# Kernel tuning notes

Hardware: AMD Instinct MI355X
Metric: run time of the kernel (lower is better)

## Reference

```python
import jax, jax.numpy as jnp
import numpy as np

B, S, D, H = 1, 1024, 1024, 16
DR, DV, R = 64, 64, 256          # rope head dim, v head dim, kv_lora_rank (qk_nope_head_dim = 0)
V, L, E, F, TOPK = 32000, 2, 4, 4096, 2
EPS, THETA, LB_WEIGHT = 1e-6, 10000.0, 0.01
SCALE = DR ** -0.5               # q_head_dim = nope(0) + rope(64)


def rms_norm(x, w):
    return x * jax.lax.rsqrt(jnp.mean(x * x, axis=-1, keepdims=True) + EPS) * w


def rotate_half(x):
    h = x.shape[-1] // 2
    return jnp.concatenate([-x[..., h:], x[..., :h]], axis=-1)


def apply_rope(x, cos, sin):
    # DeepSeek-V3 rotary: interleaved->half reorder, then rotate-half
    *lead, d = x.shape
    x = x.reshape(*lead, d // 2, 2).swapaxes(-1, -2).reshape(*lead, d)
    return x * cos + rotate_half(x) * sin


def setup_inputs() -> dict:
    key = jax.random.key(0)
    ks = iter(jax.random.split(key, 40))
    w = lambda shape: (0.02 * jax.random.normal(next(ks), shape)).astype(jnp.float32)
    return dict(
        tokens=jax.random.randint(next(ks), (B, S), 0, V, dtype=jnp.int32),
        embed=w((V, D)),                      # tied embedding / lm_head
        q_w=w((L, H * DR, D)),                # q_proj (q_lora_rank=None)
        kva_w=w((L, R + DR, D)),              # kv_a_proj_with_mqa
        kva_ln=jnp.ones((L, R), jnp.float32), # kv_a_layernorm (RMSNorm)
        kvb_w=w((L, H * DV, R)),              # kv_b_proj (nope=0 -> values only)
        o_w=w((L, D, H * DV)),
        norm1_w=jnp.ones((L, D), jnp.float32),
        norm2_w=jnp.ones((L, D), jnp.float32),
        router_w=w((L, E, D)),
        router_b=jnp.zeros((L, E), jnp.float32),
        w1=w((L, E, D, F)),
        b1=jnp.zeros((L, E, F), jnp.float32),
        w2=w((L, E, F, D)),
        b2=jnp.zeros((L, E, D), jnp.float32),
        final_norm_w=jnp.ones((D,), jnp.float32),
    )


def _layer(x, p, cos, sin, mask):
    # --- MLHA attention (DeepSeek-V3, qk_nope=0 => keys are shared rope k_pe) ---
    h = rms_norm(x, p['norm1_w'])
    q = (h @ p['q_w'].T).reshape(B, S, H, DR).transpose(0, 2, 1, 3)        # [B,H,S,DR]
    kva = h @ p['kva_w'].T                                                 # [B,S,R+DR]
    ckv, k_pe = kva[..., :R], kva[..., R:]
    v = (rms_norm(ckv, p['kva_ln']) @ p['kvb_w'].T).reshape(B, S, H, DV).transpose(0, 2, 1, 3)
    q = apply_rope(q, cos[None, None], sin[None, None])
    k = apply_rope(k_pe[:, None], cos[None, None], sin[None, None])[:, 0]  # [B,S,DR] shared across heads
    scores = jnp.einsum('bhsd,btd->bhst', q, k) * SCALE + mask
    attn = jax.nn.softmax(scores, axis=-1)
    o = jnp.einsum('bhst,bhtd->bhsd', attn, v).transpose(0, 2, 1, 3).reshape(B, S, H * DV)
    x = x + o @ p['o_w'].T
    # --- MoE FFN (top-k routing, renormalized gates, switch-style aux loss) ---
    h2 = rms_norm(x, p['norm2_w']).reshape(B * S, D)
    probs = jax.nn.softmax(h2 @ p['router_w'].T + p['router_b'], axis=-1)  # [T,E]
    topv, topi = jax.lax.top_k(probs, TOPK)
    gates = topv / jnp.sum(topv, axis=-1, keepdims=True)
    sel = jax.nn.one_hot(topi, E, dtype=probs.dtype)                       # [T,K,E]
    combine = jnp.einsum('tke,tk->te', sel, gates)                         # [T,E]
    hmid = jax.nn.gelu(jnp.einsum('td,edf->tef', h2, p['w1']) + p['b1'], approximate=False)
    y = jnp.einsum('tef,efd->ted', hmid, p['w2']) + p['b2']                # [T,E,D]
    ff = jnp.einsum('te,ted->td', combine, y).reshape(B, S, D)
    frac = jnp.mean(jnp.max(sel, axis=1), axis=0)                          # token fraction per expert
    aux = E * jnp.sum(frac * jnp.mean(probs, axis=0))
    return x + ff, aux


def reference(tokens, embed, q_w, kva_w, kva_ln, kvb_w, o_w, norm1_w, norm2_w,
              router_w, router_b, w1, b1, w2, b2, final_norm_w):
    x = embed[tokens]                                                      # [B,S,D]
    inv = 1.0 / (THETA ** (jnp.arange(0, DR, 2, dtype=jnp.float32) / DR))
    freqs = jnp.arange(S, dtype=jnp.float32)[:, None] * inv[None, :]
    emb = jnp.concatenate([freqs, freqs], axis=-1)
    cos, sin = jnp.cos(emb), jnp.sin(emb)                                  # [S,DR]
    mask = jnp.where(jnp.triu(jnp.ones((S, S), bool), 1), -jnp.inf, 0.0)[None, None]
    stacked = dict(q_w=q_w, kva_w=kva_w, kva_ln=kva_ln, kvb_w=kvb_w, o_w=o_w,
                   norm1_w=norm1_w, norm2_w=norm2_w, router_w=router_w, router_b=router_b,
                   w1=w1, b1=b1, w2=w2, b2=b2)

    def step(carry, p):
        x, aux = carry
        x, a = _layer(x, p, cos, sin, mask)
        return (x, aux + a), None

    (x, aux), _ = jax.lax.scan(step, (x, jnp.float32(0.0)), stacked)
    x = rms_norm(x, final_norm_w)
    logits = x @ embed.T                                                   # tied lm_head
    return logits, aux * LB_WEIGHT
```

## Files before the change

kernel.cpp:

```cpp
#include <hip/hip_runtime.h>
#include <hip/hip_bf16.h>
#include <math.h>

typedef __hip_bfloat16 bf16;
typedef __attribute__((ext_vector_type(8))) short short8;
typedef __attribute__((ext_vector_type(4))) short short4v;
typedef __attribute__((ext_vector_type(4))) float f32x4;

static constexpr int SEQ  = 1024;
static constexpr int DIM  = 1024;
static constexpr int NH   = 16;
static constexpr int DRR  = 64;
static constexpr int RR   = 256;
static constexpr int KVAN = RR + DRR;
static constexpr int VOC  = 32000;
static constexpr int NEXP = 4;
static constexpr int FFD  = 4096;
static constexpr int NSLOT = SEQ*2;
static constexpr float EPSF = 1e-6f;
static constexpr float ATT_SCALE = 0.125f;
static constexpr float LBW = 0.01f;

__device__ __forceinline__ bool is_bf(const uint32_t* mg){ return *mg == 0x3F803F80u; }
__device__ __forceinline__ float ldin(const void* p, size_t i, bool bf){
  return bf ? __bfloat162float(((const bf16*)p)[i]) : ((const float*)p)[i];
}
__device__ __forceinline__ short f2bs(float f){
  bf16 h = __float2bfloat16(f);
  return *reinterpret_cast<short*>(&h);
}
__device__ __forceinline__ void split2(float a, short& hi, short& lo){
  bf16 h = __float2bfloat16(a);
  hi = *reinterpret_cast<short*>(&h);
  lo = f2bs(a - __bfloat162float(h));
}

__device__ __forceinline__ void gload16(const short* gp, short* lp){
  __builtin_amdgcn_global_load_lds(
      (const __attribute__((address_space(1))) void*)gp,
      (__attribute__((address_space(3))) void*)lp, 16, 0, 0);
}

__device__ __forceinline__ void stage64(const short* __restrict__ g, int ldg,
    short* lds, int w, int lane){
  const int rA = lane >> 3;
  const int ss = (lane & 7) ^ rA;
  #pragma unroll
  for (int j = 0; j < 2; ++j){
    const int row = w*16 + j*8 + rA;
    gload16(g + (size_t)row*ldg + ss*8, lds + (w*16 + j*8)*64);
  }
}

__device__ __forceinline__ float blk_sum256(float v, float* red){
  const int tid = threadIdx.x;
  red[tid] = v; __syncthreads();
  for (int o = 128; o > 0; o >>= 1){
    if (tid < o) red[tid] += red[tid + o];
    __syncthreads();
  }
  float r = red[0]; __syncthreads();
  return r;
}
__device__ __forceinline__ float blk_max256(float v, float* red){
  const int tid = threadIdx.x;
  red[tid] = v; __syncthreads();
  for (int o = 128; o > 0; o >>= 1){
    if (tid < o) red[tid] = fmaxf(red[tid], red[tid + o]);
    __syncthreads();
  }
  float r = red[0]; __syncthreads();
  return r;
}

__global__ __launch_bounds__(256) void k_embed(const int* __restrict__ tok,
    const void* __restrict__ emb, float* __restrict__ x, const uint32_t* mg){
  const bool bf = is_bf(mg);
  const int t = blockIdx.x;
  const int id = tok[t];
  for (int d = threadIdx.x; d < DIM; d += 256)
    x[(size_t)t*DIM + d] = ldin(emb, (size_t)id*DIM + d, bf);
}

__global__ void k_ropetab(float* __restrict__ cosb, float* __restrict__ sinb){
  const int t = blockIdx.x, i = threadIdx.x;
  float inv = powf(10000.0f, -(float)i / 32.0f);
  float fr = (float)t * inv;
  cosb[t*32 + i] = cosf(fr);
  sinb[t*32 + i] = sinf(fr);
}

__global__ __launch_bounds__(256) void k_rmsnorm(const float* __restrict__ in, int instride,
    const void* __restrict__ w, size_t wofs, float* __restrict__ out, int outstride,
    int dim, const uint32_t* mg){
  __shared__ float red[256];
  const bool bf = is_bf(mg);
  const int t = blockIdx.x;
  const float* row = in + (size_t)t*instride;
  float ss = 0.f;
  for (int d = threadIdx.x; d < dim; d += 256){ float v = row[d]; ss = fmaf(v, v, ss); }
  float tot = blk_sum256(ss, red);
  float rs = rsqrtf(tot / (float)dim + EPSF);
  float* orow = out + (size_t)t*outstride;
  for (int d = threadIdx.x; d < dim; d += 256)
    orow[d] = row[d] * rs * ldin(w, wofs + d, bf);
}

__global__ __launch_bounds__(256) void k_split2_act(const float* __restrict__ X,
    short* __restrict__ S, int K, int total){
  const int i = (blockIdx.x*256 + threadIdx.x)*8;
  if (i >= total) return;
  const int row = i / K, col = i - row*K;
  const float4 v0 = *(const float4*)&X[i];
  const float4 v1 = *(const float4*)&X[i+4];
  const float vv[8] = {v0.x,v0.y,v0.z,v0.w,v1.x,v1.y,v1.z,v1.w};
  short8 h, l;
  #pragma unroll
  for (int q = 0; q < 8; ++q){ short a,b; split2(vv[q], a, b); h[q]=a; l[q]=b; }
  const size_t base = (size_t)row*2*K + col;
  *(short8*)&S[base] = h;
  *(short8*)&S[base + K] = l;
}

__global__ __launch_bounds__(256) void k_split2_wt(const void* __restrict__ W, size_t wofs,
    short* __restrict__ S, int K, int total, const uint32_t* mg){
  const bool bf = is_bf(mg);
  const int i = (blockIdx.x*256 + threadIdx.x)*8;
  if (i >= total) return;
  const int row = i / K, col = i - row*K;
  float vv[8];
  if (!bf){
    const float* Wf = (const float*)W + wofs;
    const float4 v0 = *(const float4*)&Wf[i];
    const float4 v1 = *(const float4*)&Wf[i+4];
    vv[0]=v0.x; vv[1]=v0.y; vv[2]=v0.z; vv[3]=v0.w;
    vv[4]=v1.x; vv[5]=v1.y; vv[6]=v1.z; vv[7]=v1.w;
  } else {
    #pragma unroll
    for (int q = 0; q < 8; ++q) vv[q] = __bfloat162float(((const bf16*)W)[wofs + i + q]);
  }
  short8 h, l;
  #pragma unroll
  for (int q = 0; q < 8; ++q){ short a,b; split2(vv[q], a, b); h[q]=a; l[q]=b; }
  const size_t base = (size_t)row*2*K + col;
  *(short8*)&S[base] = h;
  *(short8*)&S[base + K] = l;
}

__global__ __launch_bounds__(256) void k_split_hi(const void* __restrict__ W,
    short* __restrict__ Wh, int total, const uint32_t* mg){
  const bool bf = is_bf(mg);
  const int i = (blockIdx.x*256 + threadIdx.x)*8;
  if (i >= total) return;
  float vv[8];
  if (!bf){
    const float* Wf = (const float*)W;
    const float4 v0 = *(const float4*)&Wf[i];
    const float4 v1 = *(const float4*)&Wf[i+4];
    vv[0]=v0.x; vv[1]=v0.y; vv[2]=v0.z; vv[3]=v0.w;
    vv[4]=v1.x; vv[5]=v1.y; vv[6]=v1.z; vv[7]=v1.w;
  } else {
    #pragma unroll
    for (int q = 0; q < 8; ++q) vv[q] = __bfloat162float(((const bf16*)W)[i + q]);
  }
  short8 h;
  #pragma unroll
  for (int q = 0; q < 8; ++q) h[q] = f2bs(vv[q]);
  *(short8*)&Wh[i] = h;
}

template<int WLO>
__global__ __launch_bounds__(256) void k_transp2v(const void* __restrict__ B, size_t bofs,
    size_t perexp, short* __restrict__ S, int K, int N, const uint32_t* mg){
  __shared__ float t[64][65];
  const bool bf = is_bf(mg);
  const int e = blockIdx.z;
  const int n0 = blockIdx.x*64, k0 = blockIdx.y*64;
  const size_t src = bofs + (size_t)e*perexp;
  const int tid = threadIdx.x;
  const int rr = tid >> 4, cc = (tid & 15) * 4;
  if (!bf){
    const float* Bf = (const float*)B + src;
    #pragma unroll
    for (int p = 0; p < 4; ++p){
      const int r = rr + p*16;
      const float4 v = *(const float4*)&Bf[(size_t)(k0+r)*N + n0 + cc];
      t[r][cc+0] = v.x; t[r][cc+1] = v.y; t[r][cc+2] = v.z; t[r][cc+3] = v.w;
    }
  } else {
    #pragma unroll
    for (int p = 0; p < 4; ++p){
      const int r = rr + p*16;
      #pragma unroll
      for (int q = 0; q < 4; ++q)
        t[r][cc+q] = __bfloat162float(((const bf16*)B)[src + (size_t)(k0+r)*N + n0 + cc + q]);
    }
  }
  __syncthreads();
  const int nn = tid >> 2, ks = (tid & 3) * 16;
  const size_t dst = (size_t)e*(size_t)N*2*K + (size_t)(n0+nn)*2*K + k0 + ks;
  short8 h0, h1, l0, l1;
  #pragma unroll
  for (int q = 0; q < 8; ++q){
    short a, b;
    split2(t[ks+q][nn], a, b);      h0[q] = a; l0[q] = b;
    split2(t[ks+8+q][nn], a, b);    h1[q] = a; l1[q] = b;
  }
  *(short8*)&S[dst]     = h0;
  *(short8*)&S[dst + 8] = h1;
  if (WLO){
    *(short8*)&S[dst + K]     = l0;
    *(short8*)&S[dst + K + 8] = l1;
  }
}

__global__ __launch_bounds__(256) void k_gather2(const float* __restrict__ h2,
    const int* __restrict__ tos, short* __restrict__ S){
  const int slot = blockIdx.x, tid = threadIdx.x;
  const int t = tos[slot];
  const int i = tid*4;
  const float4 v = *(const float4*)&h2[(size_t)t*DIM + i];
  const float vv[4] = {v.x, v.y, v.z, v.w};
  short4v h, l;
  #pragma unroll
  for (int q = 0; q < 4; ++q){ short a,b; split2(vv[q], a, b); h[q]=a; l[q]=b; }
  *(short4v*)&S[(size_t)slot*2*DIM + i] = h;
  *(short4v*)&S[(size_t)slot*2*DIM + DIM + i] = l;
}

__device__ __forceinline__ void tg_stage(const short* __restrict__ A, int lda, int ac,
    const short* __restrict__ B, int ldb, int bc, int bm, int bn,
    short* sA, short* sB, int wid, int rA, int ss){
  #pragma unroll
  for (int j = 0; j < 4; ++j){
    const int row = wid*32 + j*8 + rA;
    gload16(A + (size_t)(bm+row)*lda + ac + ss*8, sA + (wid*32 + j*8)*64);
    gload16(B + (size_t)(bn+row)*ldb + bc + ss*8, sB + (wid*32 + j*8)*64);
  }
}

#define TG_MFMAS(sAp, sBp)                                                      \
    _Pragma("unroll")                                                           \
    for (int kk = 0; kk < 2; ++kk){                                             \
      short8 a[4], b[4];                                                        \
      _Pragma("unroll")                                                         \
      for (int f = 0; f < 4; ++f){                                              \
        const int ar = wr*64 + f*16 + lr;                                       \
        a[f] = *(const short8*)&(sAp)[ar*64 + (((kk*4+lks)^(ar&7)))*8];         \
        const int br = wc*64 + f*16 + lr;                                       \
        b[f] = *(const short8*)&(sBp)[br*64 + (((kk*4+lks)^(br&7)))*8];         \
      }                                                                         \
      _Pragma("unroll")                                                         \
      for (int f = 0; f < 4; ++f)                                               \
        _Pragma("unroll")                                                       \
        for (int g = 0; g < 4; ++g)                                             \
          acc[f*4+g] = __builtin_amdgcn_mfma_f32_16x16x32_bf16(                 \
              a[f], b[g], acc[f*4+g], 0, 0, 0);                                 \
    }

#define TG_KADDR(st)                                                            \
  const int kt = (st)*64;                                                       \
  const int t = (kt >= 2*K) ? 2 : (kt >= K) ? 1 : 0;                            \
  const int ko = kt - t*K;                                                      \
  const int ac = ko + ((t == 2) ? K : 0);                                       \
  const int bc = ko + ((t == 1) ? K : 0);

template<int MODE>
__global__ __launch_bounds__(256) void k_tgemm_wt(
    const short* __restrict__ A, int lda,
    const short* __restrict__ W, int ldb, int K, int nt,
    float* __restrict__ C, int N, int S, float* __restrict__ Cpart){
  __shared__ alignas(16) short sA[128*64];
  __shared__ alignas(16) short sB[128*64];
  const int tid = threadIdx.x;
  const int wid = tid >> 6, lane = tid & 63;
  const int wr = wid >> 1, wc = wid & 1;
  const int bm = blockIdx.y * 128, bn = blockIdx.x * 128;
  const int rA = lane >> 3, ss = (lane & 7) ^ rA;
  const int lr = lane & 15, lks = lane >> 4;
  f32x4 acc[16];
  #pragma unroll
  for (int i = 0; i < 16; ++i) acc[i] = f32x4{0,0,0,0};

  const int nsteps = (nt*K) >> 6;
  const int per = (nsteps + S - 1)/S;
  const int st0 = blockIdx.z*per, st1 = min(nsteps, st0 + per);
  for (int st = st0; st < st1; ++st){
    TG_KADDR(st)
    tg_stage(A, lda, ac, W, ldb, bc, bm, bn, sA, sB, wid, rA, ss);
    __syncthreads();
    TG_MFMAS(sA, sB)
    __syncthreads();
  }
  const int r4 = lks*4, cj = lr;
  if (S == 1){
    #pragma unroll
    for (int f = 0; f < 4; ++f)
      #pragma unroll
      for (int g = 0; g < 4; ++g)
        #pragma unroll
        for (int r = 0; r < 4; ++r){
          const int gm = bm + wr*64 + f*16 + r4 + r;
          const int gn = bn + wc*64 + g*16 + cj;
          if (gn >= N) continue;
          const size_t idx = (size_t)gm*N + gn;
          if (MODE == 0) C[idx] = acc[f*4+g][r];
          else           C[idx] += acc[f*4+g][r];
        }
  } else {
    const int M = gridDim.y * 128;
    float* P = Cpart + (size_t)blockIdx.z*M*N;
    #pragma unroll
    for (int f = 0; f < 4; ++f)
      #pragma unroll
      for (int g = 0; g < 4; ++g)
        #pragma unroll
        for (int r = 0; r < 4; ++r){
          const int gm = bm + wr*64 + f*16 + r4 + r;
          const int gn = bn + wc*64 + g*16 + cj;
          if (gn >= N) continue;
          P[(size_t)gm*N + gn] = acc[f*4+g][r];
        }
  }
}

__global__ __launch_bounds__(256) void k_tgemm_wtL(
    const short* __restrict__ A, int lda,
    const short* __restrict__ W, int ldb, int K,
    float* __restrict__ C, int N){
  __shared__ alignas(16) short sA[2][128*64];
  __shared__ alignas(16) short sB[2][128*64];
  const int tid = threadIdx.x;
  const int wid = tid >> 6, lane = tid & 63;
  const int wr = wid >> 1, wc = wid & 1;
  const int T = gridDim.x * gridDim.y;
  const int p = blockIdx.x + gridDim.x * blockIdx.y;
  const int u = (p & 7) * (T >> 3) + (p >> 3);
  const int bn = (u >> 3) * 128;
  const int bm = (u & 7) * 128;
  const int rA = lane >> 3, ss = (lane & 7) ^ rA;
  const int lr = lane & 15, lks = lane >> 4;
  f32x4 acc[16];
  #pragma unroll
  for (int i = 0; i < 16; ++i) acc[i] = f32x4{0,0,0,0};

  const int nsteps = K >> 6;
  tg_stage(A, lda, 0, W, ldb, 0, bm, bn, sA[0], sB[0], wid, rA, ss);
  asm volatile("s_waitcnt vmcnt(0)" ::: "memory");
  __builtin_amdgcn_s_barrier();
  int cur = 0;
  for (int st = 0; st < nsteps; ++st){
    const bool pf = (st + 1 < nsteps);
    if (pf){
      const int ko = (st + 1)*64;
      tg_stage(A, lda, ko, W, ldb, ko, bm, bn, sA[cur^1], sB[cur^1], wid, rA, ss);
    }
    __builtin_amdgcn_s_setprio(1);
    TG_MFMAS(sA[cur], sB[cur])
    __builtin_amdgcn_s_setprio(0);
    if (pf){
      asm volatile("s_waitcnt vmcnt(0)" ::: "memory");
      __builtin_amdgcn_s_barrier();
      cur ^= 1;
    }
  }
  const int r4 = lks*4, cj = lr;
  #pragma unroll
  for (int f = 0; f < 4; ++f)
    #pragma unroll
    for (int g = 0; g < 4; ++g)
      #pragma unroll
      for (int r = 0; r < 4; ++r){
        const int gm = bm + wr*64 + f*16 + r4 + r;
        const int gn = bn + wc*64 + g*16 + cj;
        if (gn >= N) continue;
        C[(size_t)gm*N + gn] = acc[f*4+g][r];
      }
}

template<int MODE>
__global__ __launch_bounds__(256) void k_redw(const float* __restrict__ Cpart,
    float* __restrict__ C, int total, int S){
  const int i = blockIdx.x*256 + threadIdx.x;
  if (i >= total) return;
  float v = 0.f;
  for (int s = 0; s < S; ++s) v += Cpart[(size_t)s*total + i];
  if (MODE == 0) C[i] = v;
  else           C[i] += v;
}

template<int ACT, int OSPLIT>
__global__ __launch_bounds__(256) void k_tgemm_grp(
    const short* __restrict__ A, int lda,
    const short* __restrict__ Wall, int ldb, int K, int nt,
    const void* __restrict__ bias, size_t biofs, size_t perexp_bias,
    float* __restrict__ Cf, short* __restrict__ Cs,
    const int* __restrict__ meta, int N, const uint32_t* mg,
    int S, float* __restrict__ Cpart){
  __shared__ alignas(16) short sA[2][128*64];
  __shared__ alignas(16) short sB[2][128*64];
  const bool bf = is_bf(mg);
  const int e = blockIdx.z / S, zs = blockIdx.z - e*S;
  const int cnt = meta[e], off = meta[NEXP + e];
  const int r0 = blockIdx.y * 128;
  if (r0 >= cnt) return;
  const int rows_valid = min(128, cnt - r0);
  const int bm = off + r0, bn = blockIdx.x * 128;
  const short* W = Wall + (size_t)e*(size_t)N*ldb;
  const size_t bib = biofs + (size_t)e * perexp_bias;

  const int tid = threadIdx.x;
  const int wid = tid >> 6, lane = tid & 63;
  const int wr = wid >> 1, wc = wid & 1;
  const int rA = lane >> 3, ss = (lane & 7) ^ rA;
  const int lr = lane & 15, lks = lane >> 4;
  f32x4 acc[16];
  #pragma unroll
  for (int i = 0; i < 16; ++i) acc[i] = f32x4{0,0,0,0};

  const int nsteps = (nt*K) >> 6;
  const int per = (nsteps + S - 1)/S;
  const int st0 = zs*per, st1 = min(nsteps, st0 + per);
  {
    TG_KADDR(st0)
    tg_stage(A, lda, ac, W, ldb, bc, bm, bn, sA[0], sB[0], wid, rA, ss);
    asm volatile("s_waitcnt vmcnt(0)" ::: "memory");
    __builtin_amdgcn_s_barrier();
  }
  int cur = 0;
  for (int st = st0; st < st1; ++st){
    const bool pf = (st + 1 < st1);
    if (pf){
      TG_KADDR(st+1)
      tg_stage(A, lda, ac, W, ldb, bc, bm, bn, sA[cur^1], sB[cur^1], wid, rA, ss);
    }
    __builtin_amdgcn_s_setprio(1);
    TG_MFMAS(sA[cur], sB[cur])
    __builtin_amdgcn_s_setprio(0);
    if (pf){
      asm volatile("s_waitcnt vmcnt(0)" ::: "memory");
      __builtin_amdgcn_s_barrier();
      cur ^= 1;
    }
  }
  const int r4 = lks*4, cj = lr;
  if (S == 1){
    #pragma unroll
    for (int f = 0; f < 4; ++f)
      #pragma unroll
      for (int g = 0; g < 4; ++g)
        #pragma unroll
        for (int r = 0; r < 4; ++r){
          const int rin = wr*64 + f*16 + r4 + r;
          if (rin >= rows_valid) continue;
          const int gn = bn + wc*64 + g*16 + cj;
          float v = acc[f*4+g][r] + ldin(bias, bib + gn, bf);
          if (ACT == 1) v = 0.5f * v * (1.f + erff(v * 0.70710678118654752f));
          if (OSPLIT){
            short hi, lo; split2(v, hi, lo);
            const size_t idx = (size_t)(bm + rin)*2*N + gn;
            Cs[idx] = hi; Cs[idx + N] = lo;
          } else {
            Cf[(size_t)(bm + rin)*N + gn] = v;
          }
        }
  } else {
    float* P = Cpart + (size_t)zs*NSLOT*N;
    #pragma unroll
    for (int f = 0; f < 4; ++f)
      #pragma unroll
      for (int g = 0; g < 4; ++g)
        #pragma unroll
        for (int r = 0; r < 4; ++r){
          const int rin = wr*64 + f*16 + r4 + r;
          if (rin >= rows_valid) continue;
          const int gn = bn + wc*64 + g*16 + cj;
          P[(size_t)(bm + rin)*N + gn] = acc[f*4+g][r];
        }
  }
}

template<int ACT, int OSPLIT>
__global__ __launch_bounds__(256) void k_tgemm_grpF(
    const short* __restrict__ A, int lda,
    const short* __restrict__ Wall, int ldb, int K,
    const void* __restrict__ bias, size_t biofs, size_t perexp_bias,
    float* __restrict__ Cf, short* __restrict__ Cs,
    const int* __restrict__ meta, int N, const uint32_t* mg,
    int S, float* __restrict__ Cpart){
  __shared__ alignas(16) short sAh[128*64];
  __shared__ alignas(16) short sAl[128*64];
  __shared__ alignas(16) short sBh[128*64];
  __shared__ alignas(16) short sBl[128*64];
  const bool bf = is_bf(mg);
  const int e = blockIdx.z / S, zs = blockIdx.z - e*S;
  const int cnt = meta[e], off = meta[NEXP + e];
  const int r0 = blockIdx.y * 128;
  if (r0 >= cnt) return;
  const int rows_valid = min(128, cnt - r0);
  const int bm = off + r0, bn = blockIdx.x * 128;
  const short* W = Wall + (size_t)e*(size_t)N*ldb;
  const size_t bib = biofs + (size_t)e * perexp_bias;

  const int tid = threadIdx.x;
  const int wid = tid >> 6, lane = tid & 63;
  const int wr = wid >> 1, wc = wid & 1;
  const int rA = lane >> 3, ss = (lane & 7) ^ rA;
  const int lr = lane & 15, lks = lane >> 4;
  f32x4 acc[16];
  #pragma unroll
  for (int i = 0; i < 16; ++i) acc[i] = f32x4{0,0,0,0};

  const int nsteps = K >> 6;
  const int per = (nsteps + S - 1)/S;
  const int st0 = zs*per, st1 = min(nsteps, st0 + per);
  for (int st = st0; st < st1; ++st){
    const int ko = st*64;
    #pragma unroll
    for (int j = 0; j < 4; ++j){
      const int row = wid*32 + j*8 + rA;
      const size_t arow = (size_t)(bm+row)*lda;
      const size_t brow = (size_t)(bn+row)*ldb;
      const int dst = (wid*32 + j*8)*64;
      gload16(A + arow + ko + ss*8,     sAh + dst);
      gload16(A + arow + K + ko + ss*8, sAl + dst);
      gload16(W + brow + ko + ss*8,     sBh + dst);
      gload16(W + brow + K + ko + ss*8, sBl + dst);
    }
    __syncthreads();
    __builtin_amdgcn_s_setprio(1);
    TG_MFMAS(sAh, sBh)
    TG_MFMAS(sAh, sBl)
    TG_MFMAS(sAl, sBh)
    __builtin_amdgcn_s_setprio(0);
    __syncthreads();
  }
  const int r4 = lks*4, cj = lr;
  if (S == 1){
    #pragma unroll
    for (int f = 0; f < 4; ++f)
      #pragma unroll
      for (int g = 0; g < 4; ++g)
        #pragma unroll
        for (int r = 0; r < 4; ++r){
          const int rin = wr*64 + f*16 + r4 + r;
          if (rin >= rows_valid) continue;
          const int gn = bn + wc*64 + g*16 + cj;
          float v = acc[f*4+g][r] + ldin(bias, bib + gn, bf);
          if (ACT == 1) v = 0.5f * v * (1.f + erff(v * 0.70710678118654752f));
          if (OSPLIT){
            short hi, lo; split2(v, hi, lo);
            const size_t idx = (size_t)(bm + rin)*2*N + gn;
            Cs[idx] = hi; Cs[idx + N] = lo;
          } else {
            Cf[(size_t)(bm + rin)*N + gn] = v;
          }
        }
  } else {
    float* P = Cpart + (size_t)zs*NSLOT*N;
    #pragma unroll
    for (int f = 0; f < 4; ++f)
      #pragma unroll
      for (int g = 0; g < 4; ++g)
        #pragma unroll
        for (int r = 0; r < 4; ++r){
          const int rin = wr*64 + f*16 + r4 + r;
          if (rin >= rows_valid) continue;
          const int gn = bn + wc*64 + g*16 + cj;
          P[(size_t)(bm + rin)*N + gn] = acc[f*4+g][r];
        }
  }
}

template<int ACT, int OSPLIT>
__global__ __launch_bounds__(256) void k_redg(const float* __restrict__ Cpart, int S,
    const int* __restrict__ eid,
    const void* __restrict__ bias, size_t biofs, size_t perexp_bias,
    float* __restrict__ Cf, short* __restrict__ Cs, int N, const uint32_t* mg){
  const bool bf = is_bf(mg);
  const int slot = blockIdx.x;
  const int e = eid[slot];
  const size_t bib = biofs + (size_t)e * perexp_bias;
  for (int n = threadIdx.x; n < N; n += 256){
    float v = 0.f;
    for (int s = 0; s < S; ++s)
      v += Cpart[(size_t)s*NSLOT*N + (size_t)slot*N + n];
    v += ldin(bias, bib + n, bf);
    if (ACT == 1) v = 0.5f * v * (1.f + erff(v * 0.70710678118654752f));
    if (OSPLIT){
      short hi, lo; split2(v, hi, lo);
      const size_t idx = (size_t)slot*2*N + n;
      Cs[idx] = hi; Cs[idx + N] = lo;
    } else {
      Cf[(size_t)slot*N + n] = v;
    }
  }
}

__global__ __launch_bounds__(512) void k_ropeq2(const float* __restrict__ qraw,
    const float* __restrict__ cosb, const float* __restrict__ sinb,
    short* __restrict__ Qsp){
  const int t = blockIdx.x, tid = threadIdx.x;
  const int hh = tid >> 5, i = tid & 31;
  const size_t base = (size_t)t*DIM + hh*DRR;
  const float u0 = qraw[base + 2*i];
  const float u1 = qraw[base + 2*i + 1];
  const float c = cosb[t*32 + i], s = sinb[t*32 + i];
  const float o0 = u0*c - u1*s;
  const float o1 = u1*c + u0*s;
  short h0,l0,h1,l1;
  split2(o0,h0,l0); split2(o1,h1,l1);
  short* q = Qsp + ((size_t)hh*SEQ + t)*128;
  q[i] = h0;      q[64+i] = l0;
  q[i+32] = h1;   q[96+i] = l1;
}

__global__ void k_ropek2(const float* __restrict__ kva,
    const float* __restrict__ cosb, const float* __restrict__ sinb,
    short* __restrict__ Kb){
  const int t = blockIdx.x, i = threadIdx.x;
  const float u0 = kva[(size_t)t*KVAN + RR + 2*i];
  const float u1 = kva[(size_t)t*KVAN + RR + 2*i + 1];
  const float c = cosb[t*32 + i], s = sinb[t*32 + i];
  const float o0 = u0*c - u1*s;
  const float o1 = u1*c + u0*s;
  short h0,l0,h1,l1;
  split2(o0,h0,l0); split2(o1,h1,l1);
  short* k = Kb + (size_t)t*128;
  k[i] = h0;      k[64+i] = l0;
  k[i+32] = h1;   k[96+i] = l1;
}

__global__ __launch_bounds__(256) void k_vsplit(const float* __restrict__ vbuf,
    short* __restrict__ Vt){
  __shared__ float tbuf[32][33];
  const int kv0 = blockIdx.x*32, d0 = blockIdx.y*32;
  const int c = threadIdx.x & 31, rb = threadIdx.x >> 5;
  #pragma unroll
  for (int p = 0; p < 4; ++p){
    const int r = rb + p*8;
    tbuf[r][c] = vbuf[(size_t)(kv0 + r)*DIM + d0 + c];
  }
  __syncthreads();
  #pragma unroll
  for (int p = 0; p < 4; ++p){
    const int rr = rb + p*8;
    const int dg = d0 + rr;
    const int h = dg >> 6, dl = dg & 63;
    short hi, lo; split2(tbuf[c][rr], hi, lo);
    const size_t o = ((size_t)h*64 + dl)*2048 + kv0 + c;
    Vt[o] = hi; Vt[o + 1024] = lo;
  }
}

__global__ __launch_bounds__(256) void k_fattn(
    const short* __restrict__ Qsp, const short* __restrict__ Kb,
    const short* __restrict__ Vt, float* __restrict__ outb){
  __shared__ alignas(16) short Qsh[64*64], Qsl[64*64];
  __shared__ alignas(16) short Ksh[64*64], Ksl[64*64];
  __shared__ alignas(16) short Vsh[64*64], Vsl[64*64];
  __shared__ alignas(16) short Ph[64*64], Pl[64*64];
  const int qt = blockIdx.x, hh = blockIdx.y;
  const int qbase = qt*64;
  const int tid = threadIdx.x;
  const int w = tid >> 6, lane = tid & 63;
  const int lr = lane & 15, lks = lane >> 4;
  const int r4 = lks*4, cj = lr;

  stage64(Qsp + ((size_t)hh*SEQ + qbase)*128,      128, Qsh, w, lane);
  stage64(Qsp + ((size_t)hh*SEQ + qbase)*128 + 64, 128, Qsl, w, lane);

  float m_r[4], l_r[4], alpha[4], rmax[4], rsum[4];
  f32x4 o[4];
  #pragma unroll
  for (int r = 0; r < 4; ++r){ m_r[r] = -3.0e38f; l_r[r] = 0.f; }
  #pragma unroll
  for (int g = 0; g < 4; ++g) o[g] = f32x4{0,0,0,0};
  __syncthreads();

  for (int kt = 0; kt <= qt; ++kt){
    const int kvbase = kt*64;
    stage64(Kb + (size_t)kvbase*128,        128, Ksh, w, lane);
    stage64(Kb + (size_t)kvbase*128 + 64,   128, Ksl, w, lane);
    stage64(Vt + (size_t)hh*64*2048 + kvbase,        2048, Vsh, w, lane);
    stage64(Vt + (size_t)hh*64*2048 + 1024 + kvbase, 2048, Vsl, w, lane);
    __syncthreads();

    f32x4 s[4];
    #pragma unroll
    for (int g = 0; g < 4; ++g) s[g] = f32x4{0,0,0,0};
    #pragma unroll
    for (int term = 0; term < 3; ++term){
      const short* Ab = (term == 2) ? Qsl : Qsh;
      const short* Bb = (term == 1) ? Ksl : Ksh;
      #pragma unroll
      for (int ks = 0; ks < 2; ++ks){
        const int arow = w*16 + lr;
        const short8 a = *(const short8*)&Ab[arow*64 + (((ks*4+lks)^(arow&7))*8)];
        #pragma unroll
        for (int g = 0; g < 4; ++g){
          const int brow = g*16 + lr;
          const short8 b = *(const short8*)&Bb[brow*64 + (((ks*4+lks)^(brow&7))*8)];
          s[g] = __builtin_amdgcn_mfma_f32_16x16x32_bf16(a, b, s[g], 0, 0, 0);
        }
      }
    }
    #pragma unroll
    for (int r = 0; r < 4; ++r) rmax[r] = -3.0e38f;
    #pragma unroll
    for (int g = 0; g < 4; ++g)
      #pragma unroll
      for (int r = 0; r < 4; ++r){
        float v = s[g][r] * ATT_SCALE;
        if (kvbase + g*16 + cj > qbase + w*16 + r4 + r) v = -3.0e38f;
        s[g][r] = v;
        rmax[r] = fmaxf(rmax[r], v);
      }
    #pragma unroll
    for (int msk = 1; msk < 16; msk <<= 1)
      #pragma unroll
      for (int r = 0; r < 4; ++r)
        rmax[r] = fmaxf(rmax[r], __shfl_xor(rmax[r], msk));
    #pragma unroll
    for (int r = 0; r < 4; ++r){
      const float mn = fmaxf(m_r[r], rmax[r]);
      alpha[r] = expf(m_r[r] - mn);
      m_r[r] = mn;
      rsum[r] = 0.f;
    }
    #pragma unroll
    for (int g = 0; g < 4; ++g)
      #pragma unroll
      for (int r = 0; r < 4; ++r){
        const float p = expf(s[g][r] - m_r[r]);
        s[g][r] = p;
        rsum[r] += p;
      }
    #pragma unroll
    for (int msk = 1; msk < 16; msk <<= 1)
      #pragma unroll
      for (int r = 0; r < 4; ++r)
        rsum[r] += __shfl_xor(rsum[r], msk);
    #pragma unroll
    for (int r = 0; r < 4; ++r)
      l_r[r] = l_r[r]*alpha[r] + rsum[r];
    #pragma unroll
    for (int g = 0; g < 4; ++g)
      #pragma unroll
      for (int r = 0; r < 4; ++r)
        o[g][r] *= alpha[r];
    #pragma unroll
    for (int g = 0; g < 4; ++g)
      #pragma unroll
      for (int r = 0; r < 4; ++r){
        short hi, lo; split2(s[g][r], hi, lo);
        const int prow = w*16 + r4 + r;
        const int sl = g*2 + (cj >> 3);
        const int addr = prow*64 + ((sl ^ (prow & 7))*8) + (cj & 7);
        Ph[addr] = hi; Pl[addr] = lo;
      }
    #pragma unroll
    for (int term = 0; term < 3; ++term){
      const short* Ab = (term == 2) ? Pl : Ph;
      const short* Bb = (term == 1) ? Vsl : Vsh;
      #pragma unroll
      for (int ks = 0; ks < 2; ++ks){
        const int arow = w*16 + lr;
        const short8 a = *(const short8*)&Ab[arow*64 + (((ks*4+lks)^(arow&7))*8)];
        #pragma unroll
        for (int g = 0; g < 4; ++g){
          const int brow = g*16 + lr;
          const short8 b = *(const short8*)&Bb[brow*64 + (((ks*4+lks)^(brow&7))*8)];
          o[g] = __builtin_amdgcn_mfma_f32_16x16x32_bf16(a, b, o[g], 0, 0, 0);
        }
      }
    }
    __syncthreads();
  }
  #pragma unroll
  for (int g = 0; g < 4; ++g)
    #pragma unroll
    for (int r = 0; r < 4; ++r)
      outb[(size_t)(qbase + w*16 + r4 + r)*DIM + hh*64 + g*16 + cj] = o[g][r] / l_r[r];
}

template<int MODE>
__global__ __launch_bounds__(256) void k_mgemm_wt(const float* __restrict__ A,
    const void* __restrict__ W, size_t wofs, float* __restrict__ C,
    int M, int N, int K, const uint32_t* mg){
  __shared__ alignas(16) short As[64][40];
  __shared__ alignas(16) short Bs[64][40];
  const bool bf = is_bf(mg);
  const int tid = threadIdx.x;
  const int bm = blockIdx.x * 64, bn = blockIdx.y * 64;
  const int wid = tid >> 6, lane = tid & 63;
  const int wr = wid >> 1, wc = wid & 1;
  const int lrow = lane & 15, lk = (lane >> 4) * 8;
  const int srow = tid >> 3, sk = (tid & 7) * 4;
  f32x4 acc00{0,0,0,0}, acc01{0,0,0,0}, acc10{0,0,0,0}, acc11{0,0,0,0};
  for (int kt = 0; kt < K; kt += 32){
    #pragma unroll
    for (int p = 0; p < 2; ++p){
      const int r = srow + p*32;
      const size_t abase = (size_t)(bm + r)*K + kt + sk;
      As[r][sk+0] = f2bs(A[abase+0]);
      As[r][sk+1] = f2bs(A[abase+1]);
      As[r][sk+2] = f2bs(A[abase+2]);
      As[r][sk+3] = f2bs(A[abase+3]);
      const size_t wbase = wofs + (size_t)(bn + r)*K + kt + sk;
      Bs[r][sk+0] = f2bs(ldin(W, wbase+0, bf));
      Bs[r][sk+1] = f2bs(ldin(W, wbase+1, bf));
      Bs[r][sk+2] = f2bs(ldin(W, wbase+2, bf));
      Bs[r][sk+3] = f2bs(ldin(W, wbase+3, bf));
    }
    __syncthreads();
    const short8 a0 = *(const short8*)&As[wr*32 +      lrow][lk];
    const short8 a1 = *(const short8*)&As[wr*32 + 16 + lrow][lk];
    const short8 b0 = *(const short8*)&Bs[wc*32 +      lrow][lk];
    const short8 b1 = *(const short8*)&Bs[wc*32 + 16 + lrow][lk];
    acc00 = __builtin_amdgcn_mfma_f32_16x16x32_bf16(a0, b0, acc00, 0, 0, 0);
    acc01 = __builtin_amdgcn_mfma_f32_16x16x32_bf16(a0, b1, acc01, 0, 0, 0);
    acc10 = __builtin_amdgcn_mfma_f32_16x16x32_bf16(a1, b0, acc10, 0, 0, 0);
    acc11 = __builtin_amdgcn_mfma_f32_16x16x32_bf16(a1, b1, acc11, 0, 0, 0);
    __syncthreads();
  }
  const int r4 = (lane >> 4) * 4, cj = lane & 15;
  #pragma unroll
  for (int fm = 0; fm < 2; ++fm)
    #pragma unroll
    for (int fn = 0; fn < 2; ++fn){
      const f32x4 av = fm == 0 ? (fn == 0 ? acc00 : acc01) : (fn == 0 ? acc10 : acc11);
      #pragma unroll
      for (int r = 0; r < 4; ++r){
        const int gm = bm + wr*32 + fm*16 + r4 + r;
        const int gn = bn + wc*32 + fn*16 + cj;
        const size_t idx = (size_t)gm*N + gn;
        if (MODE == 0) C[idx] = av[r];
        else           C[idx] += av[r];
      }
    }
}

template<int ACT>
__global__ __launch_bounds__(256) void k_gemm_grp(const float* __restrict__ A,
    const void* __restrict__ B, size_t bofs, size_t perexp_b,
    const void* __restrict__ bias, size_t biofs, size_t perexp_bias,
    float* __restrict__ C, const int* __restrict__ meta,
    int N, int K, const uint32_t* mg){
  __shared__ float As[16][68];
  __shared__ float Bs[16][68];
  const bool bf = is_bf(mg);
  const int e = blockIdx.z;
  const int cnt = meta[e], off = meta[NEXP + e];
  const int r0 = blockIdx.y * 64;
  if (r0 >= cnt) return;
  const int rows_valid = min(64, cnt - r0);
  const int bm = off + r0;
  const int bn = blockIdx.x * 64;
  const size_t bbase = bofs + (size_t)e * perexp_b;
  const size_t bibase = biofs + (size_t)e * perexp_bias;
  const int tid = threadIdx.x;
  const int tx = tid & 15, ty = tid >> 4;
  const int m0 = ty * 4, n0 = tx * 4;
  const int kcol = tid & 15, rbase = tid >> 4;
  const int nb = tid & 63, kb = tid >> 6;
  float acc[4][4];
  #pragma unroll
  for (int i = 0; i < 4; ++i)
    #pragma unroll
    for (int j = 0; j < 4; ++j) acc[i][j] = 0.f;
  for (int kt = 0; kt < K; kt += 16){
    #pragma unroll
    for (int p = 0; p < 4; ++p){
      const int r = rbase + p*16;
      As[kcol][r] = (r < rows_valid) ? A[(size_t)(bm + r)*K + kt + kcol] : 0.f;
      const int kk = kb + p*4;
      Bs[kk][nb] = ldin(B, bbase + (size_t)(kt + kk)*N + bn + nb, bf);
    }
    __syncthreads();
    #pragma unroll
    for (int kk = 0; kk < 16; ++kk){
      const float4 av = *reinterpret_cast<const float4*>(&As[kk][m0]);
      const float4 bv = *reinterpret_cast<const float4*>(&Bs[kk][n0]);
      const float aa[4] = {av.x, av.y, av.z, av.w};
      const float bb[4] = {bv.x, bv.y, bv.z, bv.w};
      #pragma unroll
      for (int i = 0; i < 4; ++i)
        #pragma unroll
        for (int j = 0; j < 4; ++j)
          acc[i][j] = fmaf(aa[i], bb[j], acc[i][j]);
    }
    __syncthreads();
  }
  #pragma unroll
  for (int i = 0; i < 4; ++i){
    const int r = m0 + i;
    if (r >= rows_valid) continue;
    #pragma unroll
    for (int j = 0; j < 4; ++j){
      const int gn = bn + n0 + j;
      float v = acc[i][j] + ldin(bias, bibase + gn, bf);
      if (ACT == 1) v = 0.5f * v * (1.f + erff(v * 0.70710678118654752f));
      C[(size_t)(bm + r)*N + gn] = v;
    }
  }
}

__global__ __launch_bounds__(512) void k_ropeq(const float* __restrict__ qraw,
    const float* __restrict__ cosb, const float* __restrict__ sinb, float* __restrict__ qro){
  const int t = blockIdx.x;
  const int tid = threadIdx.x;
  const int hh = tid >> 5, i = tid & 31;
  const size_t base = (size_t)t*DIM + hh*DRR;
  const float u0 = qraw[base + 2*i];
  const float u1 = qraw[base + 2*i + 1];
  const float c = cosb[t*32 + i], s = sinb[t*32 + i];
  qro[base + i]      = u0*c - u1*s;
  qro[base + i + 32] = u1*c + u0*s;
}

__global__ void k_ropek(const float* __restrict__ kva,
    const float* __restrict__ cosb, const float* __restrict__ sinb, float* __restrict__ kro){
  const int t = blockIdx.x, i = threadIdx.x;
  const float u0 = kva[(size_t)t*KVAN + RR + 2*i];
  const float u1 = kva[(size_t)t*KVAN + RR + 2*i + 1];
  const float c = cosb[t*32 + i], s = sinb[t*32 + i];
  kro[t*DRR + i]      = u0*c - u1*s;
  kro[t*DRR + i + 32] = u1*c + u0*s;
}

__global__ __launch_bounds__(256) void k_attn(const float* __restrict__ qro,
    const float* __restrict__ kro, const float* __restrict__ vbuf, float* __restrict__ obuf){
  __shared__ float p[SEQ];
  __shared__ float red[256];
  __shared__ float qs[DRR];
  const int s = blockIdx.x, hh = blockIdx.y, tid = threadIdx.x;
  if (tid < DRR) qs[tid] = qro[(size_t)s*DIM + hh*DRR + tid];
  __syncthreads();
  float lmax = -3.0e38f;
  for (int t = tid; t <= s; t += 256){
    const float* krow = kro + (size_t)t*DRR;
    float acc = 0.f;
    #pragma unroll
    for (int d = 0; d < DRR; ++d) acc = fmaf(qs[d], krow[d], acc);
    acc *= ATT_SCALE;
    p[t] = acc;
    lmax = fmaxf(lmax, acc);
  }
  const float m = blk_max256(lmax, red);
  float lsum = 0.f;
  for (int t = tid; t <= s; t += 256){
    const float e = expf(p[t] - m);
    p[t] = e; lsum += e;
  }
  const float den = blk_sum256(lsum, red);
  const int j = tid & 63, g = tid >> 6;
  float acc = 0.f;
  for (int t = g; t <= s; t += 4)
    acc = fmaf(p[t], vbuf[(size_t)t*DIM + hh*64 + j], acc);
  red[tid] = acc; __syncthreads();
  if (g == 0){
    const float r = red[j] + red[j+64] + red[j+128] + red[j+192];
    obuf[(size_t)s*DIM + hh*64 + j] = r / den;
  }
}

__global__ __launch_bounds__(256) void k_router(const float* __restrict__ h2,
    const void* __restrict__ rw, size_t rwofs, const void* __restrict__ rb, size_t rbofs,
    float* __restrict__ probs, int* __restrict__ topi, float* __restrict__ gates,
    const uint32_t* mg){
  __shared__ float red[256];
  const bool bf = is_bf(mg);
  const int t = blockIdx.x, tid = threadIdx.x;
  float pe[NEXP] = {0.f, 0.f, 0.f, 0.f};
  for (int d = tid; d < DIM; d += 256){
    const float hv = h2[(size_t)t*DIM + d];
    #pragma unroll
    for (int e = 0; e < NEXP; ++e) pe[e] = fmaf(hv, ldin(rw, rwofs + e*DIM + d, bf), pe[e]);
  }
  float z[NEXP];
  for (int e = 0; e < NEXP; ++e) z[e] = blk_sum256(pe[e], red);
  if (tid == 0){
    float mx = -3.0e38f;
    for (int e = 0; e < NEXP; ++e){ z[e] += ldin(rb, rbofs + e, bf); mx = fmaxf(mx, z[e]); }
    float sum = 0.f, pr[NEXP];
    for (int e = 0; e < NEXP; ++e){ pr[e] = expf(z[e] - mx); sum += pr[e]; }
    for (int e = 0; e < NEXP; ++e){ pr[e] /= sum; probs[t*NEXP + e] = pr[e]; }
    int e0 = 0;
    for (int e = 1; e < NEXP; ++e) if (pr[e] > pr[e0]) e0 = e;
    int e1 = (e0 == 0) ? 1 : 0;
    for (int e = 0; e < NEXP; ++e) if (e != e0 && pr[e] > pr[e1]) e1 = e;
    const float gs = pr[e0] + pr[e1];
    topi[t*2] = e0; topi[t*2+1] = e1;
    gates[t*2] = pr[e0]/gs; gates[t*2+1] = pr[e1]/gs;
  }
}

__global__ __launch_bounds__(256) void k_aux(const float* __restrict__ probs,
    const int* __restrict__ topi, float* __restrict__ aux, int add){
  __shared__ float red[256];
  const int tid = threadIdx.x;
  float cnt[NEXP] = {0,0,0,0}, ps[NEXP] = {0,0,0,0};
  for (int t = tid; t < SEQ; t += 256){
    cnt[topi[t*2]]   += 1.f;
    cnt[topi[t*2+1]] += 1.f;
    #pragma unroll
    for (int e = 0; e < NEXP; ++e) ps[e] += probs[t*NEXP + e];
  }
  float v = 0.f;
  for (int e = 0; e < NEXP; ++e){
    const float c  = blk_sum256(cnt[e], red);
    const float pm = blk_sum256(ps[e], red);
    v += (c / (float)SEQ) * (pm / (float)SEQ);
  }
  if (tid == 0){
    v *= (float)NEXP;
    if (add) aux[0] += v; else aux[0] = v;
  }
}

__global__ __launch_bounds__(1024) void k_assign(const int* __restrict__ topi,
    int* __restrict__ meta, int* __restrict__ sl, int* __restrict__ tos,
    int* __restrict__ eid){
  __shared__ int ti[NSLOT];
  __shared__ int cnts[NEXP];
  const int tid = threadIdx.x;
  for (int a = tid; a < NSLOT; a += 1024) ti[a] = topi[a];
  __syncthreads();
  if (tid < NEXP){
    int c = 0;
    for (int a = 0; a < NSLOT; ++a) c += (ti[a] == tid);
    cnts[tid] = c;
  }
  __syncthreads();
  int offs[NEXP];
  offs[0] = 0;
  #pragma unroll
  for (int e = 1; e < NEXP; ++e) offs[e] = offs[e-1] + cnts[e-1];
  if (tid < NEXP){ meta[tid] = cnts[tid]; meta[NEXP + tid] = offs[tid]; }
  for (int a = tid; a < NSLOT; a += 1024){
    const int e = ti[a];
    int rank = 0;
    for (int b = 0; b < a; ++b) rank += (ti[b] == e) ? 1 : 0;
    const int slot = offs[e] + rank;
    sl[a] = slot; tos[slot] = a >> 1; eid[slot] = e;
  }
}

__global__ __launch_bounds__(256) void k_gather(const float* __restrict__ h2,
    const int* __restrict__ tos, float* __restrict__ gath){
  const int slot = blockIdx.x, tid = threadIdx.x;
  const int t = tos[slot];
  #pragma unroll
  for (int ii = 0; ii < 4; ++ii)
    gath[(size_t)slot*DIM + tid + 256*ii] = h2[(size_t)t*DIM + tid + 256*ii];
}

__global__ __launch_bounds__(256) void k_combine(const float* __restrict__ y,
    const int* __restrict__ sl, const float* __restrict__ gates, float* __restrict__ x){
  const int t = blockIdx.x, tid = threadIdx.x;
  const int s0 = sl[t*2], s1 = sl[t*2+1];
  const float g0 = gates[t*2], g1 = gates[t*2+1];
  #pragma unroll
  for (int ii = 0; ii < 4; ++ii){
    const int d = tid + 256*ii;
    x[(size_t)t*DIM + d] += g0 * y[(size_t)s0*DIM + d] + g1 * y[(size_t)s1*DIM + d];
  }
}

__global__ void k_auxout(const float* __restrict__ aux, float* __restrict__ out){
  if (threadIdx.x == 0) out[0] = aux[0] * LBW;
}

extern "C" void kernel_launch(void* const* d_in, const int* in_sizes, int n_in,
                              void* d_out, int out_size, void* d_ws, size_t ws_size,
                              hipStream_t stream) {
  (void)in_sizes; (void)n_in; (void)out_size;
  const int*  tokens   = (const int*)d_in[0];
  const void* embed    = d_in[1];
  const void* q_w      = d_in[2];
  const void* kva_w    = d_in[3];
  const void* kva_ln   = d_in[4];
  const void* kvb_w    = d_in[5];
  const void* o_w      = d_in[6];
  const void* norm1_w  = d_in[7];
  const void* norm2_w  = d_in[8];
  const void* router_w = d_in[9];
  const void* router_b = d_in[10];
  const void* w1       = d_in[11];
  const void* b1       = d_in[12];
  const void* w2       = d_in[13];
  const void* b2       = d_in[14];
  const void* fnw      = d_in[15];
  const uint32_t* mg   = (const uint32_t*)kva_ln;
  float* out = (float*)d_out;

  float* ws = (float*)d_ws;
  size_t off = 0;
  auto alloc = [&](size_t n){ float* p = ws + off; off += n; return p; };
  float* x    = alloc((size_t)SEQ*DIM);
  float* h    = alloc((size_t)SEQ*DIM);
  float* qraw = alloc((size_t)SEQ*DIM);
  float* qro  = alloc((size_t)SEQ*DIM);
  float* kva  = alloc((size_t)SEQ*KVAN);
  float* ckvn = alloc((size_t)SEQ*RR);
  float* kro  = alloc((size_t)SEQ*DRR);
  float* vbuf = alloc((size_t)SEQ*DIM);
  float* cosb = alloc((size_t)SEQ*32);
  float* sinb = alloc((size_t)SEQ*32);
  float* probs= alloc((size_t)SEQ*NEXP);
  float* gates= alloc((size_t)SEQ*2);
  int*   topi = (int*)alloc((size_t)SEQ*2);
  float* aux  = alloc(8);
  int*   meta = (int*)alloc(16);
  int*   sl   = (int*)alloc(NSLOT);
  int*   tos  = (int*)alloc(NSLOT);
  int*   eid  = (int*)alloc(NSLOT);
  float* ybuf = alloc((size_t)NSLOT*DIM);
  short* hsp  = (short*)alloc((size_t)SEQ*DIM);
  short* dwsp = (short*)alloc((size_t)DIM*DIM);
  float* gslab  = alloc((size_t)NSLOT*DIM);
  short* gsp  = (short*)gslab;
  float* hmslab = alloc((size_t)NSLOT*FFD);
  short* hmsp = (short*)hmslab;
  short* Qsp = (short*)alloc((size_t)NH*SEQ*64);
  short* Kb  = (short*)alloc((size_t)SEQ*64);
  short* Vt  = (short*)alloc((size_t)NH*64*1024);
  const size_t wt_elems = (size_t)NEXP*DIM*FFD;
  const bool useT = (off + wt_elems) * sizeof(float) <= ws_size;
  short* mosp = nullptr;
  if (useT){ float* slab = alloc(wt_elems); mosp = (short*)slab; }
  const size_t emb_elems = (size_t)VOC*DIM;
  const bool useE = useT && (off + emb_elems/2) * sizeof(float) <= ws_size;
  short* embh = nullptr;
  if (useE){ embh = (short*)alloc(emb_elems/2); }
  const size_t part_elems = (size_t)4*SEQ*DIM;
  const bool useS = useT && (off + part_elems) * sizeof(float) <= ws_size;
  float* part = nullptr;
  if (useS){ part = alloc(part_elems); }

  const int Sd  = useS ? 4 : 1;
  const int Sg2 = useS ? 2 : 1;

  k_embed<<<SEQ, 256, 0, stream>>>(tokens, embed, x, mg);
  k_ropetab<<<SEQ, 32, 0, stream>>>(cosb, sinb);
  if (useE)
    k_split_hi<<<(int)(emb_elems/2048), 256, 0, stream>>>(embed, embh, (int)emb_elems, mg);

  for (int l = 0; l < 2; ++l){
    k_rmsnorm<<<SEQ, 256, 0, stream>>>(x, DIM, norm1_w, (size_t)l*DIM, h, DIM, DIM, mg);
    k_split2_act<<<SEQ*DIM/2048, 256, 0, stream>>>(h, hsp, DIM, SEQ*DIM);
    k_split2_wt<<<DIM*DIM/2048, 256, 0, stream>>>(q_w, (size_t)l*DIM*DIM, dwsp, DIM, DIM*DIM, mg);
    k_tgemm_wt<0><<<dim3(DIM/128, SEQ/128, Sd), 256, 0, stream>>>(
        hsp, 2*DIM, dwsp, 2*DIM, DIM, 3, qraw, DIM, Sd, part);
    if (Sd > 1) k_redw<0><<<(SEQ*DIM+255)/256, 256, 0, stream>>>(part, qraw, SEQ*DIM, Sd);
    k_split2_wt<<<KVAN*DIM/2048, 256, 0, stream>>>(kva_w, (size_t)l*KVAN*DIM, dwsp, DIM, KVAN*DIM, mg);
    k_tgemm_wt<0><<<dim3((KVAN+127)/128, SEQ/128, Sd), 256, 0, stream>>>(
        hsp, 2*DIM, dwsp, 2*DIM, DIM, 3, kva, KVAN, Sd, part);
    if (Sd > 1) k_redw<0><<<(SEQ*KVAN+255)/256, 256, 0, stream>>>(part, kva, SEQ*KVAN, Sd);
    k_rmsnorm<<<SEQ, 256, 0, stream>>>(kva, KVAN, kva_ln, (size_t)l*RR, ckvn, RR, RR, mg);
    k_split2_act<<<SEQ*RR/2048, 256, 0, stream>>>(ckvn, hsp, RR, SEQ*RR);
    k_split2_wt<<<DIM*RR/2048, 256, 0, stream>>>(kvb_w, (size_t)l*DIM*RR, dwsp, RR, DIM*RR, mg);
    k_tgemm_wt<0><<<dim3(DIM/128, SEQ/128, Sd), 256, 0, stream>>>(
        hsp, 2*RR, dwsp, 2*RR, RR, 3, vbuf, DIM, Sd, part);
    if (Sd > 1) k_redw<0><<<(SEQ*DIM+255)/256, 256, 0, stream>>>(part, vbuf, SEQ*DIM, Sd);
    if (useT){
      k_ropeq2<<<SEQ, 512, 0, stream>>>(qraw, cosb, sinb, Qsp);
      k_ropek2<<<SEQ, 32, 0, stream>>>(kva, cosb, sinb, Kb);
      k_vsplit<<<dim3(SEQ/32, DIM/32), 256, 0, stream>>>(vbuf, Vt);
      k_fattn<<<dim3(SEQ/64, NH), 256, 0, stream>>>(Qsp, Kb, Vt, qraw);
    } else {
      k_ropeq<<<SEQ, 512, 0, stream>>>(qraw, cosb, sinb, qro);
      k_ropek<<<SEQ, 32, 0, stream>>>(kva, cosb, sinb, kro);
      k_attn<<<dim3(SEQ, NH), 256, 0, stream>>>(qro, kro, vbuf, qraw);
    }
    k_split2_act<<<SEQ*DIM/2048, 256, 0, stream>>>(qraw, hsp, DIM, SEQ*DIM);
    k_split2_wt<<<DIM*DIM/2048, 256, 0, stream>>>(o_w, (size_t)l*DIM*DIM, dwsp, DIM, DIM*DIM, mg);
    k_tgemm_wt<1><<<dim3(DIM/128, SEQ/128, Sd), 256, 0, stream>>>(
        hsp, 2*DIM, dwsp, 2*DIM, DIM, 3, x, DIM, Sd, part);
    if (Sd > 1) k_redw<1><<<(SEQ*DIM+255)/256, 256, 0, stream>>>(part, x, SEQ*DIM, Sd);
    k_rmsnorm<<<SEQ, 256, 0, stream>>>(x, DIM, norm2_w, (size_t)l*DIM, h, DIM, DIM, mg);
    k_router<<<SEQ, 256, 0, stream>>>(h, router_w, (size_t)l*NEXP*DIM,
                                      router_b, (size_t)l*NEXP, probs, topi, gates, mg);
    k_aux<<<1, 256, 0, stream>>>(probs, topi, aux, l);
    k_assign<<<1, 1024, 0, stream>>>(topi, meta, sl, tos, eid);
    if (useT){
      k_gather2<<<NSLOT, 256, 0, stream>>>(h, tos, gsp);
      if (l == 0){
        k_transp2v<1><<<dim3(FFD/64, DIM/64, NEXP), 256, 0, stream>>>(
            w1, (size_t)l*NEXP*DIM*FFD, (size_t)DIM*FFD, mosp, DIM, FFD, mg);
        k_tgemm_grpF<1,1><<<dim3(FFD/128, NSLOT/128, NEXP), 256, 0, stream>>>(
            gsp, 2*DIM, mosp, 2*DIM, DIM,
            b1, (size_t)l*NEXP*FFD, (size_t)FFD, nullptr, hmsp, meta, FFD, mg, 1, nullptr);
        k_transp2v<1><<<dim3(DIM/64, FFD/64, NEXP), 256, 0, stream>>>(
            w2, (size_t)l*NEXP*FFD*DIM, (size_t)FFD*DIM, mosp, FFD, DIM, mg);
        k_tgemm_grpF<0,0><<<dim3(DIM/128, NSLOT/128, NEXP*Sg2), 256, 0, stream>>>(
            hmsp, 2*FFD, mosp, 2*FFD, FFD,
            b2, (size_t)l*NEXP*DIM, (size_t)DIM, ybuf, nullptr, meta, DIM, mg, Sg2, part);
      } else {
        k_transp2v<0><<<dim3(FFD/64, DIM/64, NEXP), 256, 0, stream>>>(
            w1, (size_t)l*NEXP*DIM*FFD, (size_t)DIM*FFD, mosp, DIM, FFD, mg);
        k_tgemm_grp<1,1><<<dim3(FFD/128, NSLOT/128, NEXP), 256, 0, stream>>>(
            gsp, 2*DIM, mosp, 2*DIM, DIM, 1,
            b1, (size_t)l*NEXP*FFD, (size_t)FFD, nullptr, hmsp, meta, FFD, mg, 1, nullptr);
        k_transp2v<0><<<dim3(DIM/64, FFD/64, NEXP), 256, 0, stream>>>(
            w2, (size_t)l*NEXP*FFD*DIM, (size_t)FFD*DIM, mosp, FFD, DIM, mg);
        k_tgemm_grp<0,0><<<dim3(DIM/128, NSLOT/128, NEXP*Sg2), 256, 0, stream>>>(
            hmsp, 2*FFD, mosp, 2*FFD, FFD, 1,
            b2, (size_t)l*NEXP*DIM, (size_t)DIM, ybuf, nullptr, meta, DIM, mg, Sg2, part);
      }
      if (Sg2 > 1)
        k_redg<0,0><<<NSLOT, 256, 0, stream>>>(part, Sg2, eid,
            b2, (size_t)l*NEXP*DIM, (size_t)DIM, ybuf, nullptr, DIM, mg);
    } else {
      k_gather<<<NSLOT, 256, 0, stream>>>(h, tos, gslab);
      k_gemm_grp<1><<<dim3(FFD/64, NSLOT/64, NEXP), 256, 0, stream>>>(
          gslab, w1, (size_t)l*NEXP*DIM*FFD, (size_t)DIM*FFD,
          b1, (size_t)l*NEXP*FFD, (size_t)FFD, hmslab, meta, FFD, DIM, mg);
      k_gemm_grp<0><<<dim3(DIM/64, NSLOT/64, NEXP), 256, 0, stream>>>(
          hmslab, w2, (size_t)l*NEXP*FFD*DIM, (size_t)FFD*DIM,
          b2, (size_t)l*NEXP*DIM, (size_t)DIM, ybuf, meta, DIM, FFD, mg);
    }
    k_combine<<<SEQ, 256, 0, stream>>>(ybuf, sl, gates, x);
  }

  k_rmsnorm<<<SEQ, 256, 0, stream>>>(x, DIM, fnw, 0, h, DIM, DIM, mg);
  if (useE){
    k_split2_act<<<SEQ*DIM/2048, 256, 0, stream>>>(h, hsp, DIM, SEQ*DIM);
    k_tgemm_wtL<<<dim3(VOC/128, SEQ/128), 256, 0, stream>>>(
        hsp, 2*DIM, embh, DIM, DIM, out, VOC);
  } else {
    k_mgemm_wt<0><<<dim3(SEQ/64, VOC/64), 256, 0, stream>>>(
        h, embed, 0, out, SEQ, VOC, DIM, mg);
  }
  k_auxout<<<1, 1, 0, stream>>>(aux, out + (size_t)SEQ*VOC);
}
```

Baseline: 1.350 ms.

## Enlarge lm_head GEMM tiles to 256x256 with 512-thread blocks

The tied lm_head GEMM kernel moves from 128x128 tiles with 4 waves to 256x256 tiles with 8 waves. Each wave now computes a 128x64 output block, which halves global traffic per output element and raises MFMA work per LDS read. The XCD-aware block remapping is rewritten to handle a tile count that is not a multiple of 8. In exchange each block uses 128 KB of LDS and 128 accumulator registers per lane. Occupancy drops, and the grid of 125x4 = 500 blocks gives a coarser tail across compute units.

```diff
diff --git a/kernel.cpp b/kernel.cpp
--- a/kernel.cpp
+++ b/kernel.cpp
@@ -324,39 +324,66 @@
   }
 }
 
-__global__ __launch_bounds__(256) void k_tgemm_wtL(
+__global__ __launch_bounds__(512, 2) void k_tgemm_wtL(
     const short* __restrict__ A, int lda,
     const short* __restrict__ W, int ldb, int K,
     float* __restrict__ C, int N){
-  __shared__ alignas(16) short sA[2][128*64];
-  __shared__ alignas(16) short sB[2][128*64];
+  __shared__ alignas(16) short sA[2][256*64];
+  __shared__ alignas(16) short sB[2][256*64];
   const int tid = threadIdx.x;
   const int wid = tid >> 6, lane = tid & 63;
-  const int wr = wid >> 1, wc = wid & 1;
+  const int wr = wid >> 2, wc = wid & 3;
   const int T = gridDim.x * gridDim.y;
   const int p = blockIdx.x + gridDim.x * blockIdx.y;
-  const int u = (p & 7) * (T >> 3) + (p >> 3);
-  const int bn = (u >> 3) * 128;
-  const int bm = (u & 7) * 128;
+  const int xcd = p & 7, idx = p >> 3;
+  const int q = T >> 3, r = T & 7;
+  const int u = ((xcd < r) ? xcd*(q+1) : r*(q+1) + (xcd-r)*q) + idx;
+  const int bn = (u >> 2) * 256;
+  const int bm = (u & 3) * 256;
   const int rA = lane >> 3, ss = (lane & 7) ^ rA;
   const int lr = lane & 15, lks = lane >> 4;
-  f32x4 acc[16];
-  #pragma unroll
-  for (int i = 0; i < 16; ++i) acc[i] = f32x4{0,0,0,0};
+  f32x4 acc[32];
+  #pragma unroll
+  for (int i = 0; i < 32; ++i) acc[i] = f32x4{0,0,0,0};
+
+  auto stage = [&](int ko, int buf){
+    #pragma unroll
+    for (int j = 0; j < 4; ++j){
+      const int row = wid*32 + j*8 + rA;
+      gload16(A + (size_t)(bm+row)*lda + ko + ss*8, sA[buf] + (wid*32 + j*8)*64);
+      gload16(W + (size_t)(bn+row)*ldb + ko + ss*8, sB[buf] + (wid*32 + j*8)*64);
+    }
+  };
 
   const int nsteps = K >> 6;
-  tg_stage(A, lda, 0, W, ldb, 0, bm, bn, sA[0], sB[0], wid, rA, ss);
+  stage(0, 0);
   asm volatile("s_waitcnt vmcnt(0)" ::: "memory");
   __builtin_amdgcn_s_barrier();
   int cur = 0;
   for (int st = 0; st < nsteps; ++st){
     const bool pf = (st + 1 < nsteps);
-    if (pf){
-      const int ko = (st + 1)*64;
-      tg_stage(A, lda, ko, W, ldb, ko, bm, bn, sA[cur^1], sB[cur^1], wid, rA, ss);
-    }
+    if (pf) stage((st + 1)*64, cur^1);
     __builtin_amdgcn_s_setprio(1);
-    TG_MFMAS(sA[cur], sB[cur])
+    #pragma unroll
+    for (int kk = 0; kk < 2; ++kk){
+      short8 a[8], b[4];
+      #pragma unroll
+      for (int f = 0; f < 8; ++f){
+        const int ar = wr*128 + f*16 + lr;
+        a[f] = *(const short8*)&sA[cur][ar*64 + (((kk*4+lks)^(ar&7)))*8];
+      }
+      #pragma unroll
+      for (int g = 0; g < 4; ++g){
+        const int br = wc*64 + g*16 + lr;
+        b[g] = *(const short8*)&sB[cur][br*64 + (((kk*4+lks)^(br&7)))*8];
+      }
+      #pragma unroll
+      for (int f = 0; f < 8; ++f)
+        #pragma unroll
+        for (int g = 0; g < 4; ++g)
+          acc[f*4+g] = __builtin_amdgcn_mfma_f32_16x16x32_bf16(
+              a[f], b[g], acc[f*4+g], 0, 0, 0);
+    }
     __builtin_amdgcn_s_setprio(0);
     if (pf){
       asm volatile("s_waitcnt vmcnt(0)" ::: "memory");
@@ -366,15 +393,15 @@
   }
   const int r4 = lks*4, cj = lr;
   #pragma unroll
-  for (int f = 0; f < 4; ++f)
+  for (int f = 0; f < 8; ++f)
     #pragma unroll
     for (int g = 0; g < 4; ++g)
       #pragma unroll
-      for (int r = 0; r < 4; ++r){
-        const int gm = bm + wr*64 + f*16 + r4 + r;
+      for (int rr = 0; rr < 4; ++rr){
+        const int gm = bm + wr*128 + f*16 + r4 + rr;
         const int gn = bn + wc*64 + g*16 + cj;
         if (gn >= N) continue;
-        C[(size_t)gm*N + gn] = acc[f*4+g][r];
+        C[(size_t)gm*N + gn] = acc[f*4+g][rr];
       }
 }
 
@@ -1227,7 +1254,7 @@
   k_rmsnorm<<<SEQ, 256, 0, stream>>>(x, DIM, fnw, 0, h, DIM, DIM, mg);
   if (useE){
     k_split2_act<<<SEQ*DIM/2048, 256, 0, stream>>>(h, hsp, DIM, SEQ*DIM);
-    k_tgemm_wtL<<<dim3(VOC/128, SEQ/128), 256, 0, stream>>>(
+    k_tgemm_wtL<<<dim3(VOC/256, SEQ/256), 512, 0, stream>>>(
         hsp, 2*DIM, embh, DIM, DIM, out, VOC);
   } else {
     k_mgemm_wt<0><<<dim3(SEQ/64, VOC/64), 256, 0, stream>>>(
```

Result: faster. 1.323 ms (-2.0%).
